# Kernel tuning notes

Measured on AMD Instinct MI355X. Metric: run time of the kernel, lower is better.

The kernel has to match this reference:

```python
import jax, jax.numpy as jnp
import numpy as np

B, N, C, H = 8, 1024, 768, 12
D = C // H
HID = 4 * C
MAX_TEXT_LEN = 512
LN_EPS = 1e-5


def _ln(x, g, b):
    mu = jnp.mean(x, axis=-1, keepdims=True)
    var = jnp.mean(jnp.square(x - mu), axis=-1, keepdims=True)
    return (x - mu) * jax.lax.rsqrt(var + LN_EPS) * g + b


def _mlp(x, w1, b1, w2, b2):
    h = jax.nn.gelu(x @ w1.T + b1, approximate=False)
    return h @ w2.T + b2


def setup_inputs() -> dict:
    key = jax.random.key(0)
    ks = jax.random.split(key, 16)
    s = 0.02
    return {
        "x": jax.random.normal(ks[0], (B, N, C), jnp.float32),
        "mask": jax.random.randint(ks[1], (B, N), 0, 2).astype(bool),
        "rel_bias": jax.random.normal(ks[2], (H, N, N), jnp.float32) * s,
        "w_qkv": jax.random.normal(ks[3], (3 * C, C), jnp.float32) * s,
        "q_bias": jnp.zeros((C,), jnp.float32),
        "v_bias": jnp.zeros((C,), jnp.float32),
        "w_proj": jax.random.normal(ks[4], (C, C), jnp.float32) * s,
        "b_proj": jnp.zeros((C,), jnp.float32),
        "ln1_g": jnp.ones((C,), jnp.float32),
        "ln1_b": jnp.zeros((C,), jnp.float32),
        "ln2t_g": jnp.ones((C,), jnp.float32),
        "ln2t_b": jnp.zeros((C,), jnp.float32),
        "ln2i_g": jnp.ones((C,), jnp.float32),
        "ln2i_b": jnp.zeros((C,), jnp.float32),
        "w1t": jax.random.normal(ks[5], (HID, C), jnp.float32) * s,
        "b1t": jnp.zeros((HID,), jnp.float32),
        "w2t": jax.random.normal(ks[6], (C, HID), jnp.float32) * s,
        "b2t": jnp.zeros((C,), jnp.float32),
        "w1i": jax.random.normal(ks[7], (HID, C), jnp.float32) * s,
        "b1i": jnp.zeros((HID,), jnp.float32),
        "w2i": jax.random.normal(ks[8], (C, HID), jnp.float32) * s,
        "b2i": jnp.zeros((C,), jnp.float32),
        "gamma1": jnp.full((C,), 0.1, jnp.float32),
        "gamma2": jnp.full((C,), 0.1, jnp.float32),
    }


def reference(x, mask, rel_bias, w_qkv, q_bias, v_bias, w_proj, b_proj,
              ln1_g, ln1_b, ln2t_g, ln2t_b, ln2i_g, ln2i_b,
              w1t, b1t, w2t, b2t, w1i, b1i, w2i, b2i, gamma1, gamma2):
    # ---- attention branch ----
    h = _ln(x, ln1_g, ln1_b)
    qkv_bias = jnp.concatenate([q_bias, jnp.zeros_like(v_bias), v_bias])
    qkv = h @ w_qkv.T + qkv_bias                      # [B,N,3C]
    qkv = qkv.reshape(B, N, 3, H, D).transpose(2, 0, 3, 1, 4)  # [3,B,H,N,D]
    q, k, v = qkv[0], qkv[1], qkv[2]
    q = q * (D ** -0.5)
    attn = jnp.einsum('bhnd,bhmd->bhnm',
                      q.astype(jnp.float32), k.astype(jnp.float32))
    attn = attn + rel_bias[None]                      # [B,H,N,N]
    attn = jnp.where(mask[:, None, None, :], attn, -jnp.inf)
    attn = jax.nn.softmax(attn, axis=-1).astype(x.dtype)
    out = jnp.einsum('bhnm,bhmd->bhnd', attn, v)
    out = out.transpose(0, 2, 1, 3).reshape(B, N, C)
    out = out @ w_proj.T + b_proj
    x = x + gamma1 * out
    # ---- dual-branch layer-scaled MLP (mlp_vl is None path) ----
    xt = x[:, :MAX_TEXT_LEN]
    xi = x[:, MAX_TEXT_LEN:]
    xt = xt + gamma2 * _mlp(_ln(xt, ln2t_g, ln2t_b), w1t, b1t, w2t, b2t)
    xi = xi + gamma2 * _mlp(_ln(xi, ln2i_g, ln2i_b), w1i, b1i, w2i, b2i)
    return jnp.concatenate([xt, xi], axis=1)
```

## Files before the change

### kernel.cpp

```cpp
#include <hip/hip_runtime.h>
#include <hip/hip_bf16.h>
#include <math.h>

#define B_    8
#define N_TOK 1024
#define C_    768
#define H_    12
#define D_    64
#define HID_  3072

typedef __attribute__((ext_vector_type(4)))  float f32x4;
typedef __attribute__((ext_vector_type(16))) float f32x16;
typedef __attribute__((ext_vector_type(8)))  short s16x8;
typedef __attribute__((ext_vector_type(4)))  unsigned short u16x4;

static __device__ __forceinline__ unsigned short f2bf(float x){
  union { __hip_bfloat16 h; unsigned short u; } cv;
  cv.h = __float2bfloat16(x);
  return cv.u;
}
static __device__ __forceinline__ float bf2f(unsigned short u){
  return __uint_as_float(((unsigned)u) << 16);
}

#define GLOAD_LDS16(gp, lp) \
  __builtin_amdgcn_global_load_lds((const __attribute__((address_space(1))) unsigned int*)(gp), \
                                   (__attribute__((address_space(3))) unsigned int*)(lp), 16, 0, 0)

__global__ __launch_bounds__(256) void k_cvtall(
    const float* __restrict__ wq,  const float* __restrict__ wp,
    const float* __restrict__ w1t, const float* __restrict__ w2t,
    const float* __restrict__ w1i, const float* __restrict__ w2i,
    const float* __restrict__ bias,
    unsigned short* __restrict__ dq,  unsigned short* __restrict__ dp,
    unsigned short* __restrict__ d1t, unsigned short* __restrict__ d2t,
    unsigned short* __restrict__ d1i, unsigned short* __restrict__ d2i,
    unsigned short* __restrict__ db,
    const float* __restrict__ x,
    const float* __restrict__ ln1g, const float* __restrict__ ln1b,
    unsigned short* __restrict__ hln)
{
  if (blockIdx.x >= 23808){
    int row  = (blockIdx.x - 23808)*4 + (threadIdx.x >> 6);
    int lane = threadIdx.x & 63;
    const float* xr = x + (size_t)row*C_;
    float v[12]; float s = 0.f;
    #pragma unroll
    for (int i=0;i<12;i++){ v[i] = xr[lane + i*64]; s += v[i]; }
    #pragma unroll
    for (int m=1;m<64;m<<=1) s += __shfl_xor(s, m);
    float mu = s * (1.f/768.f);
    float vs = 0.f;
    #pragma unroll
    for (int i=0;i<12;i++){ float d = v[i]-mu; vs += d*d; }
    #pragma unroll
    for (int m=1;m<64;m<<=1) vs += __shfl_xor(vs, m);
    float rs = rsqrtf(vs*(1.f/768.f) + 1e-5f);
    unsigned short* orow = hln + (size_t)row*C_;
    #pragma unroll
    for (int i=0;i<12;i++){ int c = lane + i*64; orow[c] = f2bf((v[i]-mu)*rs*ln1g[c] + ln1b[c]); }
    return;
  }
  int i = blockIdx.x * 256 + threadIdx.x;
  const float* src; unsigned short* dst; int o;
  if      (i <  442368){ src = wq;  dst = dq;  o = i; }
  else if (i <  589824){ src = wp;  dst = dp;  o = i -  442368; }
  else if (i < 1179648){ src = w1t; dst = d1t; o = i -  589824; }
  else if (i < 1769472){ src = w2t; dst = d2t; o = i - 1179648; }
  else if (i < 2359296){ src = w1i; dst = d1i; o = i - 1769472; }
  else if (i < 2949120){ src = w2i; dst = d2i; o = i - 2359296; }
  else                 { src = bias;dst = db;  o = i - 2949120; }
  float4 v = ((const float4*)src)[o];
  u16x4 r;
  r.x = f2bf(v.x); r.y = f2bf(v.y); r.z = f2bf(v.z); r.w = f2bf(v.w);
  *(u16x4*)(dst + (size_t)o*4) = r;
}

__global__ __launch_bounds__(256) void k_ln2(const float* __restrict__ xmid,
                                             const float* __restrict__ gt, const float* __restrict__ bt,
                                             const float* __restrict__ gi, const float* __restrict__ bi,
                                             unsigned short* __restrict__ outc){
  int row  = blockIdx.x*4 + (threadIdx.x >> 6);
  int lane = threadIdx.x & 63;
  int bb = row >> 10, n = row & 1023;
  const float* G = (n < 512) ? gt : gi;
  const float* Bb = (n < 512) ? bt : bi;
  int crow = (n < 512) ? (bb*512 + n) : (4096 + bb*512 + (n - 512));
  const float* xr = xmid + (size_t)row*C_;
  float v[12]; float s = 0.f;
  #pragma unroll
  for (int i=0;i<12;i++){ v[i] = xr[lane + i*64]; s += v[i]; }
  #pragma unroll
  for (int m=1;m<64;m<<=1) s += __shfl_xor(s, m);
  float mu = s * (1.f/768.f);
  float vs = 0.f;
  #pragma unroll
  for (int i=0;i<12;i++){ float d = v[i]-mu; vs += d*d; }
  #pragma unroll
  for (int m=1;m<64;m<<=1) vs += __shfl_xor(vs, m);
  float rs = rsqrtf(vs*(1.f/768.f) + 1e-5f);
  unsigned short* orow = outc + (size_t)crow*C_;
  #pragma unroll
  for (int i=0;i<12;i++){ int c = lane + i*64; orow[c] = f2bf((v[i]-mu)*rs*G[c] + Bb[c]); }
}

template<int MODE, int TM>
__global__ __launch_bounds__(TM==256 ? 512 : 256, TM==256 ? 2 : 3) void k_gemm2(
    const unsigned short* __restrict__ A,
    const unsigned short* __restrict__ Bw0,
    const unsigned short* __restrict__ Bw1,
    int K,
    const float* __restrict__ bias0,
    const float* __restrict__ bias1,
    const float* __restrict__ qb2,
    const float* __restrict__ resid,
    const float* __restrict__ gamma,
    unsigned short* __restrict__ out_bf,
    float* __restrict__ out_f)
{
  constexpr int THREADS = (TM == 256) ? 512 : 256;
  constexpr int ASLOT = TM * 64;
  constexpr int SLOT  = ASLOT + 8192;
  constexpr int BITS  = 8192 / (THREADS * 16);
  __shared__ __align__(16) char smem[3 * SLOT];
  const int tid = threadIdx.x;
  const int lane = tid & 63, w = tid >> 6;
  const int wr = w >> 1, wc = w & 1;
  const int l31 = lane & 31, h5 = lane >> 5;

  const int gx = gridDim.x, gy = gridDim.y;
  const int nwg = gx * gy;
  const int flat = blockIdx.y * gx + blockIdx.x;
  const int nid = (flat & 7) * (nwg >> 3) + (flat >> 3);
  const int by = nid % gy, bx = nid / gy;
  const int z = blockIdx.z;
  const int row0 = bx*TM, col0 = by*128;

  const unsigned short* Ap = A;
  const unsigned short* Bp = Bw0;
  const float* bias = bias0;
  if (MODE == 2 || MODE == 3){
    if (z){ Ap = A + (size_t)4096*K; Bp = Bw1; bias = bias1; }
  }
  const char* Abase = (const char*)Ap;
  const char* Bbase = (const char*)Bp;
  const size_t rowbytes = (size_t)K*2;
  const int KT2 = K >> 5;

  auto stage = [&](int h, int slot_idx){
    char* slot = smem + slot_idx*SLOT;
    size_t kb = (size_t)h*64;
    #pragma unroll
    for (int it = 0; it < 2; it++){
      int L = it*(THREADS*16) + tid*16;
      int r = L >> 6, cb = L & 63;
      GLOAD_LDS16(Abase + (size_t)(row0 + r)*rowbytes + kb + (cb ^ ((r & 6) << 3)), slot + L);
    }
    #pragma unroll
    for (int it = 0; it < BITS; it++){
      int L = it*(THREADS*16) + tid*16;
      int r = L >> 6, cb = L & 63;
      GLOAD_LDS16(Bbase + (size_t)(col0 + r)*rowbytes + kb + (cb ^ ((r & 6) << 3)), slot + ASLOT + L);
    }
  };

  stage(0, 0); stage(1, 1);
  if constexpr (TM == 256) asm volatile("s_waitcnt vmcnt(3)" ::: "memory");
  else                     asm volatile("s_waitcnt vmcnt(4)" ::: "memory");
  __builtin_amdgcn_s_barrier();

  f32x16 acc[2][2] = {};
  int sh = 2, sc_ = 0;
  for (int h = 0; h < KT2; h++){
    if (h + 2 < KT2){
      stage(h + 2, sh);
      sh = (sh == 2) ? 0 : sh + 1;
    }
    char* slot = smem + sc_*SLOT;
    sc_ = (sc_ == 2) ? 0 : sc_ + 1;
    s16x8 af[2][2], bfr[2][2];
    #pragma unroll
    for (int fm = 0; fm < 2; fm++){
      int ra = wr*64 + fm*32 + l31;
      int swa = (ra & 6) << 3;
      af[fm][0] = *(const s16x8*)(slot + ra*64 + ((h5*16) ^ swa));
      af[fm][1] = *(const s16x8*)(slot + ra*64 + ((32 + h5*16) ^ swa));
    }
    #pragma unroll
    for (int fn = 0; fn < 2; fn++){
      int rb = wc*64 + fn*32 + l31;
      int swb = (rb & 6) << 3;
      bfr[fn][0] = *(const s16x8*)(slot + ASLOT + rb*64 + ((h5*16) ^ swb));
      bfr[fn][1] = *(const s16x8*)(slot + ASLOT + rb*64 + ((32 + h5*16) ^ swb));
    }
    __builtin_amdgcn_s_setprio(1);
    #pragma unroll
    for (int kh = 0; kh < 2; kh++)
      #pragma unroll
      for (int fm = 0; fm < 2; fm++)
        #pragma unroll
        for (int fn = 0; fn < 2; fn++)
          acc[fm][fn] = __builtin_amdgcn_mfma_f32_32x32x16_bf16(af[fm][kh], bfr[fn][kh], acc[fm][fn], 0, 0, 0);
    __builtin_amdgcn_s_setprio(0);
    if (h + 1 < KT2){
      if (h + 2 < KT2){
        if constexpr (TM == 256) asm volatile("s_waitcnt vmcnt(3)" ::: "memory");
        else                     asm volatile("s_waitcnt vmcnt(4)" ::: "memory");
      } else {
        asm volatile("s_waitcnt vmcnt(0)" ::: "memory");
      }
      __builtin_amdgcn_s_barrier();
    }
  }

  #pragma unroll
  for (int fm = 0; fm < 2; fm++){
    #pragma unroll
    for (int fn = 0; fn < 2; fn++){
      int j = col0 + wc*64 + fn*32 + l31;
      f32x16 a = acc[fm][fn];
      if (MODE == 0){
        int which = (j >= 1536) ? 2 : (j >= 768 ? 1 : 0);
        int cj = j - which*768;
        float bs = (which == 0) ? bias0[cj] : (which == 2 ? qb2[cj] : 0.f);
        int head = cj >> 6, d = cj & 63;
        #pragma unroll
        for (int r = 0; r < 16; r++){
          int m = row0 + wr*64 + fm*32 + (r & 3) + 8*(r >> 2) + 4*h5;
          int bb = m >> 10, n = m & 1023;
          float val = a[r] + bs;
          if (which == 0) val *= 0.125f;
          out_bf[((((size_t)which*B_ + bb)*H_ + head)*N_TOK + n)*D_ + d] = f2bf(val);
        }
      } else if (MODE == 1){
        float gm = gamma[j], bs = bias[j];
        #pragma unroll
        for (int r = 0; r < 16; r++){
          int m = row0 + wr*64 + fm*32 + (r & 3) + 8*(r >> 2) + 4*h5;
          size_t idx = (size_t)m*C_ + j;
          out_f[idx] = resid[idx] + gm*(a[r] + bs);
        }
      } else if (MODE == 2){
        float bs = bias[j];
        unsigned short* outp = out_bf + (size_t)z*4096*HID_;
        #pragma unroll
        for (int r = 0; r < 16; r++){
          int m = row0 + wr*64 + fm*32 + (r & 3) + 8*(r >> 2) + 4*h5;
          float t = a[r] + bs;
          outp[(size_t)m*HID_ + j] = f2bf(0.5f*t*(1.f + erff(t*0.70710678118654752f)));
        }
      } else {
        float gm = gamma[j], bs = bias[j];
        #pragma unroll
        for (int r = 0; r < 16; r++){
          int m = row0 + wr*64 + fm*32 + (r & 3) + 8*(r >> 2) + 4*h5;
          int bb = m >> 9, n = (m & 511) + (z ? 512 : 0);
          size_t idx = ((size_t)bb*N_TOK + n)*C_ + j;
          out_f[idx] = resid[idx] + gm*(a[r] + bs);
        }
      }
    }
  }
}

__global__ __launch_bounds__(256, 2) void k_attn(
    const unsigned short* __restrict__ qb,
    const unsigned short* __restrict__ kb,
    const unsigned short* __restrict__ vb,
    const unsigned short* __restrict__ bias_bf,
    const int* __restrict__ mask,
    unsigned short* __restrict__ outb)
{
  __shared__ __align__(16) char smem[45056];
  char* Vt0 = smem;
  char* Vt1 = smem + 8192;
  char* Ks  = smem + 16384;
  char* Bs  = smem + 24576;
  float* maskf = (float*)(smem + 40960);
  char* Oep = smem;

  int wg = blockIdx.x;
  int x = wg & 7, rest = wg >> 3;
  int qt = rest & 7, gl = rest >> 3;
  int g = gl*8 + x;
  int h = g % 12, bb = g / 12;

  const int tid = threadIdx.x, lane = tid & 63, w = tid >> 6;
  const int l31 = lane & 31, h5 = lane >> 5;
  const size_t bh = (size_t)bb*H_ + h;
  const char* qp = (const char*)(qb + bh*N_TOK*D_);
  const char* kp = (const char*)(kb + bh*N_TOK*D_);
  const unsigned short* vp = vb + bh*N_TOK*D_;
  const char* bp = (const char*)(bias_bf + (size_t)h*N_TOK*N_TOK);
  const int q0 = qt*128;
  const int qrow = q0 + w*32 + l31;
  const int qr = w*32 + l31;

  #pragma unroll
  for (int it = 0; it < 2; it++){
    int L = it*4096 + tid*16; int r = L >> 7, cb = L & 127;
    GLOAD_LDS16(kp + (size_t)r*128 + (cb ^ ((r & 7) << 4)), Ks + L);
  }
  #pragma unroll
  for (int it = 0; it < 4; it++){
    int L = it*4096 + tid*16; int r = L >> 7, cb = L & 127;
    GLOAD_LDS16(bp + (size_t)(q0 + r)*2048 + (cb ^ ((r & 7) << 4)), Bs + L);
  }
  unsigned short vv[16];
  #pragma unroll
  for (int j = 0; j < 16; j++) vv[j] = vp[(size_t)(w*16 + j)*D_ + lane];
  {
    int4 m4 = *(const int4*)(mask + bb*N_TOK + tid*4);
    float4 f4;
    f4.x = m4.x ? 0.f : -1e30f; f4.y = m4.y ? 0.f : -1e30f;
    f4.z = m4.z ? 0.f : -1e30f; f4.w = m4.w ? 0.f : -1e30f;
    *(float4*)(maskf + tid*4) = f4;
  }
  s16x8 qf[4];
  #pragma unroll
  for (int t = 0; t < 4; t++)
    qf[t] = *(const s16x8*)(qp + (size_t)qrow*128 + t*32 + h5*16);
  #pragma unroll
  for (int i = 0; i < 2; i++){
    s16x8 pk;
    #pragma unroll
    for (int e = 0; e < 8; e++) pk[e] = (short)vv[i*8 + e];
    *(s16x8*)(Vt0 + lane*128 + ((w*32 + i*16) ^ ((lane & 7) << 4))) = pk;
  }
  __syncthreads();

  f32x16 oacc[2] = {};
  float lrow = 0.f;

  for (int t = 0; t < 16; t++){
    const int kt = t*64;
    char* Vbuf = (t & 1) ? Vt1 : Vt0;
    char* Vnxt = (t & 1) ? Vt0 : Vt1;

    s16x8 kfr[2][4];
    #pragma unroll
    for (int ck = 0; ck < 2; ck++)
      #pragma unroll
      for (int tt = 0; tt < 4; tt++)
        kfr[ck][tt] = *(const s16x8*)(Ks + (ck*32 + l31)*128 + ((tt*32 + h5*16) ^ ((l31 & 7) << 4)));
    u16x4 bv[2][4];
    #pragma unroll
    for (int ck = 0; ck < 2; ck++)
      #pragma unroll
      for (int rq = 0; rq < 4; rq++){
        int off = ck*64 + rq*16 + h5*8;
        bv[ck][rq] = *(const u16x4*)(Bs + qr*128 + (off ^ ((qr & 7) << 4)));
      }
    __syncthreads();

    if (t < 15){
      #pragma unroll
      for (int it = 0; it < 2; it++){
        int L = it*4096 + tid*16; int r = L >> 7, cb = L & 127;
        GLOAD_LDS16(kp + (size_t)(kt + 64 + r)*128 + (cb ^ ((r & 7) << 4)), Ks + L);
      }
      #pragma unroll
      for (int it = 0; it < 4; it++){
        int L = it*4096 + tid*16; int r = L >> 7, cb = L & 127;
        GLOAD_LDS16(bp + (size_t)(q0 + r)*2048 + (size_t)(kt + 64)*2 + (cb ^ ((r & 7) << 4)), Bs + L);
      }
      #pragma unroll
      for (int j = 0; j < 16; j++)
        vv[j] = vp[(size_t)(kt + 64 + w*16 + j)*D_ + lane];
    }

    f32x16 sacc[2] = {};
    __builtin_amdgcn_s_setprio(1);
    #pragma unroll
    for (int tt = 0; tt < 4; tt++){
      sacc[0] = __builtin_amdgcn_mfma_f32_32x32x16_bf16(kfr[0][tt], qf[tt], sacc[0], 0, 0, 0);
      sacc[1] = __builtin_amdgcn_mfma_f32_32x32x16_bf16(kfr[1][tt], qf[tt], sacc[1], 0, 0, 0);
    }
    __builtin_amdgcn_s_setprio(0);

    float sv[2][16];
    float ps = 0.f;
    #pragma unroll
    for (int ck = 0; ck < 2; ck++){
      #pragma unroll
      for (int r = 0; r < 16; r++){
        int kk = ck*32 + (r & 3) + 8*(r >> 2) + 4*h5;
        float p = __expf(sacc[ck][r] + bf2f(bv[ck][r >> 2][r & 3]) + maskf[kt + kk]);
        sv[ck][r] = p;
        ps += p;
      }
    }
    lrow += ps;

    #pragma unroll
    for (int ck = 0; ck < 2; ck++){
      #pragma unroll
      for (int kh = 0; kh < 2; kh++){
        unsigned wA, wB, wC, wD;
        asm("v_cvt_pk_bf16_f32 %0, %1, %2" : "=v"(wA) : "v"(sv[ck][kh*8+0]), "v"(sv[ck][kh*8+1]));
        asm("v_cvt_pk_bf16_f32 %0, %1, %2" : "=v"(wB) : "v"(sv[ck][kh*8+2]), "v"(sv[ck][kh*8+3]));
        asm("v_cvt_pk_bf16_f32 %0, %1, %2" : "=v"(wC) : "v"(sv[ck][kh*8+4]), "v"(sv[ck][kh*8+5]));
        asm("v_cvt_pk_bf16_f32 %0, %1, %2" : "=v"(wD) : "v"(sv[ck][kh*8+6]), "v"(sv[ck][kh*8+7]));
        unsigned tA = (unsigned)__shfl_xor((int)wA, 32);
        unsigned tB = (unsigned)__shfl_xor((int)wB, 32);
        unsigned tC = (unsigned)__shfl_xor((int)wC, 32);
        unsigned tD = (unsigned)__shfl_xor((int)wD, 32);
        union { unsigned u[4]; s16x8 v; } pu;
        pu.u[0] = h5 ? tC : wA;
        pu.u[1] = h5 ? tD : wB;
        pu.u[2] = h5 ? wC : tA;
        pu.u[3] = h5 ? wD : tB;
        __builtin_amdgcn_s_setprio(1);
        #pragma unroll
        for (int dt = 0; dt < 2; dt++){
          int d = dt*32 + l31;
          s16x8 vf = *(const s16x8*)(Vbuf + d*128 + ((ck*64 + kh*32 + h5*16) ^ ((d & 7) << 4)));
          oacc[dt] = __builtin_amdgcn_mfma_f32_32x32x16_bf16(vf, pu.v, oacc[dt], 0, 0, 0);
        }
        __builtin_amdgcn_s_setprio(0);
      }
    }

    if (t < 15){
      #pragma unroll
      for (int i = 0; i < 2; i++){
        s16x8 pk;
        #pragma unroll
        for (int e = 0; e < 8; e++) pk[e] = (short)vv[i*8 + e];
        *(s16x8*)(Vnxt + lane*128 + ((w*32 + i*16) ^ ((lane & 7) << 4))) = pk;
      }
    }
    __syncthreads();
  }

  lrow += __shfl_xor(lrow, 32);
  float inv = 1.f / lrow;
  char* Ow = Oep + w*8192;
  #pragma unroll
  for (int dt = 0; dt < 2; dt++)
    #pragma unroll
    for (int r = 0; r < 16; r++){
      int d = dt*32 + (r & 3) + 8*(r >> 2) + 4*h5;
      *(float*)(Ow + l31*256 + ((d*4) ^ ((l31 & 7) << 4))) = oacc[dt][r] * inv;
    }
  int q2 = lane >> 1, dh = lane & 1;
  float of[32];
  #pragma unroll
  for (int i = 0; i < 8; i++){
    f32x4 v4 = *(const f32x4*)(Ow + q2*256 + ((dh*128 + i*16) ^ ((q2 & 7) << 4)));
    of[i*4+0] = v4[0]; of[i*4+1] = v4[1]; of[i*4+2] = v4[2]; of[i*4+3] = v4[3];
  }
  unsigned short* orow = outb + ((size_t)bb*N_TOK + q0 + w*32 + q2)*C_ + h*64 + dh*32;
  #pragma unroll
  for (int i = 0; i < 4; i++){
    s16x8 ob;
    #pragma unroll
    for (int e = 0; e < 8; e++) ob[e] = (short)f2bf(of[i*8+e]);
    *(s16x8*)(orow + i*8) = ob;
  }
}

extern "C" void kernel_launch(void* const* d_in, const int* in_sizes, int n_in,
                              void* d_out, int out_size, void* d_ws, size_t ws_size,
                              hipStream_t stream) {
  const float* x      = (const float*)d_in[0];
  const int*   mask   = (const int*)  d_in[1];
  const float* relb   = (const float*)d_in[2];
  const float* w_qkv  = (const float*)d_in[3];
  const float* q_bias = (const float*)d_in[4];
  const float* v_bias = (const float*)d_in[5];
  const float* w_proj = (const float*)d_in[6];
  const float* b_proj = (const float*)d_in[7];
  const float* ln1_g  = (const float*)d_in[8];
  const float* ln1_b  = (const float*)d_in[9];
  const float* ln2t_g = (const float*)d_in[10];
  const float* ln2t_b = (const float*)d_in[11];
  const float* ln2i_g = (const float*)d_in[12];
  const float* ln2i_b = (const float*)d_in[13];
  const float* w1t    = (const float*)d_in[14];
  const float* b1t    = (const float*)d_in[15];
  const float* w2t    = (const float*)d_in[16];
  const float* b2t    = (const float*)d_in[17];
  const float* w1i    = (const float*)d_in[18];
  const float* b1i    = (const float*)d_in[19];
  const float* w2i    = (const float*)d_in[20];
  const float* b2i    = (const float*)d_in[21];
  const float* gamma1 = (const float*)d_in[22];
  const float* gamma2 = (const float*)d_in[23];
  float* out = (float*)d_out;
  char* ws = (char*)d_ws;

  size_t off = 0;
  auto nxt = [&](size_t b){ size_t r = off; off += (b + 255) & ~(size_t)255; return r; };
  unsigned short* wq_bf  = (unsigned short*)(ws + nxt((size_t)3*C_*C_*2));
  unsigned short* wp_bf  = (unsigned short*)(ws + nxt((size_t)C_*C_*2));
  unsigned short* w1t_bf = (unsigned short*)(ws + nxt((size_t)HID_*C_*2));
  unsigned short* w2t_bf = (unsigned short*)(ws + nxt((size_t)HID_*C_*2));
  unsigned short* w1i_bf = (unsigned short*)(ws + nxt((size_t)HID_*C_*2));
  unsigned short* w2i_bf = (unsigned short*)(ws + nxt((size_t)HID_*C_*2));
  unsigned short* hln    = (unsigned short*)(ws + nxt((size_t)B_*N_TOK*C_*2));
  unsigned short* qkv    = (unsigned short*)(ws + nxt((size_t)3*B_*N_TOK*C_*2));
  unsigned short* attno  = (unsigned short*)(ws + nxt((size_t)B_*N_TOK*C_*2));
  float*          xmid   = (float*)(ws + nxt((size_t)B_*N_TOK*C_*4));
  unsigned short* ln2c   = hln;
  unsigned short* hidden = qkv;
  unsigned short* bias_bf = (unsigned short*)xmid;

  k_cvtall<<<dim3(25856), 256, 0, stream>>>(w_qkv, w_proj, w1t, w2t, w1i, w2i, relb,
                                            wq_bf, wp_bf, w1t_bf, w2t_bf, w1i_bf, w2i_bf, bias_bf,
                                            x, ln1_g, ln1_b, hln);

  k_gemm2<0,256><<<dim3(32, 18, 1), 512, 0, stream>>>(hln, wq_bf, nullptr, C_,
                                                      q_bias, nullptr, v_bias,
                                                      nullptr, nullptr, qkv, nullptr);

  const size_t qsz = (size_t)B_*H_*N_TOK*D_;
  k_attn<<<dim3(768), 256, 0, stream>>>(qkv, qkv + qsz, qkv + 2*qsz, bias_bf, mask, attno);

  k_gemm2<1,128><<<dim3(64, 6, 1), 256, 0, stream>>>(attno, wp_bf, nullptr, C_,
                                                     b_proj, nullptr, nullptr,
                                                     x, gamma1, nullptr, xmid);

  k_ln2<<<dim3(B_*N_TOK/4), 256, 0, stream>>>(xmid, ln2t_g, ln2t_b, ln2i_g, ln2i_b, ln2c);

  k_gemm2<2,256><<<dim3(16, 24, 2), 512, 0, stream>>>(ln2c, w1t_bf, w1i_bf, C_,
                                                      b1t, b1i, nullptr,
                                                      nullptr, nullptr, hidden, nullptr);

  k_gemm2<3,128><<<dim3(32, 6, 2), 256, 0, stream>>>(hidden, w2t_bf, w2i_bf, HID_,
                                                     b2t, b2i, nullptr,
                                                     xmid, gamma2, nullptr, out);
}
```

Measured before the change: 304.8 us.

## Add 256x256-tile GEMM kernel with phased LDS pipeline for QKV and FC1

Adds a new k_gemm8 kernel that computes 256x256 output tiles with 8 waves. It uses a 128KB double-buffered swizzled LDS layout, direct global-to-LDS loads interleaved with MFMA phases, s_setprio, and an XCD-aware block remap. The QKV projection and the FC1+GELU GEMMs switch to this kernel with half as many column blocks, aiming for more operand reuse and better load/compute overlap. The 128KB of LDS per block limits occupancy to one block per CU, and the kernel hardcodes K=768.

Result: slower. 345.3 us (+13.3%).

```diff
diff --git a/kernel.cpp b/kernel.cpp
--- a/kernel.cpp
+++ b/kernel.cpp
@@ -102,6 +102,133 @@
   unsigned short* orow = outc + (size_t)crow*C_;
   #pragma unroll
   for (int i=0;i<12;i++){ int c = lane + i*64; orow[c] = f2bf((v[i]-mu)*rs*G[c] + Bb[c]); }
+}
+
+template<int MODE>
+__global__ __launch_bounds__(512, 2) void k_gemm8(
+    const unsigned short* __restrict__ A,
+    const unsigned short* __restrict__ Bw0,
+    const unsigned short* __restrict__ Bw1,
+    const float* __restrict__ bias0,
+    const float* __restrict__ bias1,
+    const float* __restrict__ qb2,
+    unsigned short* __restrict__ out_bf)
+{
+  __shared__ __align__(16) char smem[131072];
+  const int tid = threadIdx.x;
+  const int lane = tid & 63, w = tid >> 6;
+  const int wr = w >> 2, wc = w & 3;
+  const int l31 = lane & 31, h5 = lane >> 5;
+
+  const int gx = gridDim.x, gy = gridDim.y;
+  const int nwg = gx * gy;
+  const int flat = blockIdx.y * gx + blockIdx.x;
+  const int nid = (flat & 7) * (nwg >> 3) + (flat >> 3);
+  const int by = nid % gy, bx = nid / gy;
+  const int z = blockIdx.z;
+  const int row0 = bx*256, col0 = by*256;
+
+  const unsigned short* Ap = A;
+  const unsigned short* Bp = Bw0;
+  const float* bias = bias0;
+  if (MODE == 2){
+    if (z){ Ap = A + (size_t)4096*C_; Bp = Bw1; bias = bias1; }
+  }
+  const char* Abase = (const char*)Ap;
+  const char* Bbase = (const char*)Bp;
+  const size_t rowbytes = (size_t)C_*2;
+
+  auto stage_half = [&](int kt, int which){
+    char* dst = smem + (kt & 1)*65536 + ((which & 2) ? 32768 : 0) + (which & 1)*16384;
+    const char* srcb = (which & 2) ? Bbase : Abase;
+    int rowbase = ((which & 2) ? col0 : row0) + (which & 1)*128;
+    size_t kb = (size_t)kt*128;
+    #pragma unroll
+    for (int it = 0; it < 2; it++){
+      int L = it*8192 + tid*16;
+      int r = L >> 7, cb = L & 127;
+      GLOAD_LDS16(srcb + (size_t)(rowbase + r)*rowbytes + kb + (cb ^ ((r & 7) << 4)), dst + L);
+    }
+  };
+
+  f32x16 acc[4][2] = {};
+
+#define PHASE8(BUFOFS, MH, NH, SKT, SW) { \
+    s16x8 af0[4], af1[4], bfq[4]; \
+    int ra0 = wr*128 + (MH)*64 + l31;  int swa0 = (ra0 & 7) << 4; \
+    int ra1 = ra0 + 32;                int swa1 = (ra1 & 7) << 4; \
+    int rb  = wc*64 + (NH)*32 + l31;   int swb  = (rb & 7) << 4; \
+    _Pragma("unroll") \
+    for (int ks = 0; ks < 4; ks++){ \
+      af0[ks] = *(const s16x8*)(smem + (BUFOFS) + ra0*128 + ((ks*32 + h5*16) ^ swa0)); \
+      af1[ks] = *(const s16x8*)(smem + (BUFOFS) + ra1*128 + ((ks*32 + h5*16) ^ swa1)); \
+      bfq[ks] = *(const s16x8*)(smem + (BUFOFS) + 32768 + rb*128 + ((ks*32 + h5*16) ^ swb)); \
+    } \
+    if ((SKT) < 12) stage_half((SKT), (SW)); \
+    __builtin_amdgcn_s_barrier(); \
+    __builtin_amdgcn_s_setprio(1); \
+    _Pragma("unroll") \
+    for (int ks = 0; ks < 4; ks++){ \
+      acc[(MH)*2+0][NH] = __builtin_amdgcn_mfma_f32_32x32x16_bf16(af0[ks], bfq[ks], acc[(MH)*2+0][NH], 0, 0, 0); \
+      acc[(MH)*2+1][NH] = __builtin_amdgcn_mfma_f32_32x32x16_bf16(af1[ks], bfq[ks], acc[(MH)*2+1][NH], 0, 0, 0); \
+    } \
+    __builtin_amdgcn_s_setprio(0); \
+  }
+
+  stage_half(0, 0); stage_half(0, 1); stage_half(0, 2); stage_half(0, 3);
+  asm volatile("s_waitcnt vmcnt(0)" ::: "memory");
+  __builtin_amdgcn_s_barrier();
+
+  for (int i = 0; i < 6; i++){
+    const int ka1 = 2*i + 1, ka2 = 2*i + 2;
+    PHASE8(0, 0, 0, ka1, 0);
+    PHASE8(0, 0, 1, ka1, 1);
+    PHASE8(0, 1, 0, ka1, 2);
+    PHASE8(0, 1, 1, ka1, 3);
+    asm volatile("s_waitcnt vmcnt(0)" ::: "memory");
+    __builtin_amdgcn_s_barrier();
+    PHASE8(65536, 0, 0, ka2, 0);
+    PHASE8(65536, 0, 1, ka2, 1);
+    PHASE8(65536, 1, 0, ka2, 2);
+    PHASE8(65536, 1, 1, ka2, 3);
+    if (i < 5){
+      asm volatile("s_waitcnt vmcnt(0)" ::: "memory");
+      __builtin_amdgcn_s_barrier();
+    }
+  }
+#undef PHASE8
+
+  #pragma unroll
+  for (int fm = 0; fm < 4; fm++){
+    #pragma unroll
+    for (int fn = 0; fn < 2; fn++){
+      int j = col0 + wc*64 + fn*32 + l31;
+      f32x16 a = acc[fm][fn];
+      if (MODE == 0){
+        int which = (j >= 1536) ? 2 : (j >= 768 ? 1 : 0);
+        int cj = j - which*768;
+        float bs = (which == 0) ? bias0[cj] : (which == 2 ? qb2[cj] : 0.f);
+        int head = cj >> 6, d = cj & 63;
+        #pragma unroll
+        for (int r = 0; r < 16; r++){
+          int m = row0 + wr*128 + fm*32 + (r & 3) + 8*(r >> 2) + 4*h5;
+          int bb = m >> 10, n = m & 1023;
+          float val = a[r] + bs;
+          if (which == 0) val *= 0.125f;
+          out_bf[((((size_t)which*B_ + bb)*H_ + head)*N_TOK + n)*D_ + d] = f2bf(val);
+        }
+      } else {
+        float bs = bias[j];
+        unsigned short* outp = out_bf + (size_t)z*4096*HID_;
+        #pragma unroll
+        for (int r = 0; r < 16; r++){
+          int m = row0 + wr*128 + fm*32 + (r & 3) + 8*(r >> 2) + 4*h5;
+          float t = a[r] + bs;
+          outp[(size_t)m*HID_ + j] = f2bf(0.5f*t*(1.f + erff(t*0.70710678118654752f)));
+        }
+      }
+    }
+  }
 }
 
 template<int MODE, int TM>
@@ -510,9 +637,8 @@
                                             wq_bf, wp_bf, w1t_bf, w2t_bf, w1i_bf, w2i_bf, bias_bf,
                                             x, ln1_g, ln1_b, hln);
 
-  k_gemm2<0,256><<<dim3(32, 18, 1), 512, 0, stream>>>(hln, wq_bf, nullptr, C_,
-                                                      q_bias, nullptr, v_bias,
-                                                      nullptr, nullptr, qkv, nullptr);
+  k_gemm8<0><<<dim3(32, 9, 1), 512, 0, stream>>>(hln, wq_bf, nullptr,
+                                                 q_bias, nullptr, v_bias, qkv);
 
   const size_t qsz = (size_t)B_*H_*N_TOK*D_;
   k_attn<<<dim3(768), 256, 0, stream>>>(qkv, qkv + qsz, qkv + 2*qsz, bias_bf, mask, attno);
@@ -523,9 +649,8 @@
 
   k_ln2<<<dim3(B_*N_TOK/4), 256, 0, stream>>>(xmid, ln2t_g, ln2t_b, ln2i_g, ln2i_b, ln2c);
 
-  k_gemm2<2,256><<<dim3(16, 24, 2), 512, 0, stream>>>(ln2c, w1t_bf, w1i_bf, C_,
-                                                      b1t, b1i, nullptr,
-                                                      nullptr, nullptr, hidden, nullptr);
+  k_gemm8<2><<<dim3(16, 12, 2), 512, 0, stream>>>(ln2c, w1t_bf, w1i_bf,
+                                                  b1t, b1i, nullptr, hidden);
 
   k_gemm2<3,128><<<dim3(32, 6, 2), 256, 0, stream>>>(hidden, w2t_bf, w2i_bf, HID_,
                                                      b2t, b2i, nullptr,
```
